# Performance work log

Hardware: AMD Instinct MI355X
Metric: run time of the kernel (lower is better)

Reference implementation:

```python
import jax, jax.numpy as jnp
import numpy as np

B, T, C = 2, 2048, 1024
H = 16
D = C // H  # head_dim = 64
SCALE = D ** -0.5


def setup_inputs() -> dict:
    key = jax.random.key(0)
    ks = jax.random.split(key, 5)
    s = 0.02
    return {
        "x": jax.random.normal(ks[0], (B, T, C), dtype=jnp.float32),
        "w_qkv": jax.random.normal(ks[1], (C, 3 * C), dtype=jnp.float32) * s,
        "b_qkv": jnp.zeros((3 * C,), dtype=jnp.float32),
        "w_proj": jax.random.normal(ks[2], (C, C), dtype=jnp.float32) * s,
        "b_proj": jnp.zeros((C,), dtype=jnp.float32),
    }


def reference(x, w_qkv, b_qkv, w_proj, b_proj):
    Bx, Tx, Cx = x.shape
    qkv = x @ w_qkv + b_qkv                      # [B,T,3C]
    q, k, v = jnp.split(qkv, 3, axis=-1)
    # [B,T,C] -> [B,H,T,D]
    q = q.reshape(Bx, Tx, H, D).transpose(0, 2, 1, 3)
    k = k.reshape(Bx, Tx, H, D).transpose(0, 2, 1, 3)
    v = v.reshape(Bx, Tx, H, D).transpose(0, 2, 1, 3)
    attn = jnp.einsum('bhqd,bhkd->bhqk', q, k) * SCALE
    causal = jnp.tril(jnp.ones((Tx, Tx), dtype=bool))
    attn = jnp.where(causal[None, None], attn, -jnp.inf)
    attn = jax.nn.softmax(attn, axis=-1)
    out = jnp.einsum('bhqk,bhkd->bhqd', attn, v)  # [B,H,T,D]
    out = out.transpose(0, 2, 1, 3).reshape(Bx, Tx, Cx)
    return out @ w_proj + b_proj
```

## Files before the change

### kernel.cpp

```cpp
#include <hip/hip_runtime.h>
#include <hip/hip_bf16.h>
#include <math.h>

#define T_SEQ 2048
#define NHEAD 16
#define HDIM  64
#define CDIM  1024
#define KDIM  1024
#define SCALE_L2E 0.1803368801111204f

typedef __attribute__((ext_vector_type(8))) short bf16x8;
typedef __attribute__((ext_vector_type(4))) float f32x4;
typedef __attribute__((ext_vector_type(16))) float f32x16;
typedef __attribute__((ext_vector_type(8))) unsigned short u16x8;
typedef __attribute__((ext_vector_type(4))) unsigned int u32x4;

__device__ __forceinline__ unsigned short f2bf(float f) {
    unsigned int u = __builtin_bit_cast(unsigned int, f);
    u += 0x7fffu + ((u >> 16) & 1u);
    return (unsigned short)(u >> 16);
}
__device__ __forceinline__ unsigned int cvt_pk_bf16(float lo, float hi_) {
    unsigned int r;
    asm("v_cvt_pk_bf16_f32 %0, %1, %2" : "=v"(r) : "v"(lo), "v"(hi_));
    return r;
}
__device__ __forceinline__ void pl32swap(unsigned int &a, unsigned int &b) {
    asm("v_permlane32_swap_b32 %0, %1" : "+v"(a), "+v"(b));
}
__device__ __forceinline__ float exp2_fast(float x) {
    float r; asm("v_exp_f32 %0, %1" : "=v"(r) : "v"(x)); return r;
}
__device__ __forceinline__ void gld16(const unsigned short* g, unsigned short* l) {
    __builtin_amdgcn_global_load_lds(
        (const __attribute__((address_space(1))) unsigned int*)g,
        (__attribute__((address_space(3))) unsigned int*)l,
        16, 0, 0);
}

__global__ __launch_bounds__(256) void prep_all(
    const float* __restrict__ x,  unsigned short* __restrict__ Xb,
    const float* __restrict__ wq, unsigned short* __restrict__ Wqt,
    const float* __restrict__ wp, unsigned short* __restrict__ Wpt)
{
    __shared__ unsigned short Ls[64][72];
    const int bid = blockIdx.x;
    if (bid < 2048) {
        size_t i = ((size_t)bid * 256 + threadIdx.x) * 8;
        float4 a = *(const float4*)(x + i);
        float4 b = *(const float4*)(x + i + 4);
        u32x4 o;
        o[0] = cvt_pk_bf16(a.x, a.y);
        o[1] = cvt_pk_bf16(a.z, a.w);
        o[2] = cvt_pk_bf16(b.x, b.y);
        o[3] = cvt_pk_bf16(b.z, b.w);
        *(u32x4*)(Xb + i) = o;
        return;
    }
    const float* W; unsigned short* Wt; int NC, n0, k0;
    if (bid < 2048 + 768) {
        int b = bid - 2048;
        W = wq; Wt = Wqt; NC = 3072; n0 = (b % 48) * 64; k0 = (b / 48) * 64;
    } else {
        int b = bid - 2816;
        W = wp; Wt = Wpt; NC = 1024; n0 = (b % 16) * 64; k0 = (b / 16) * 64;
    }
    const int t = threadIdx.x;
    {
        int kr = t >> 2, nc = (t & 3) * 16;
        #pragma unroll
        for (int j = 0; j < 4; j++) {
            float4 v = *(const float4*)(W + (size_t)(k0 + kr) * NC + n0 + nc + j * 4);
            Ls[nc + j*4 + 0][kr] = f2bf(v.x);
            Ls[nc + j*4 + 1][kr] = f2bf(v.y);
            Ls[nc + j*4 + 2][kr] = f2bf(v.z);
            Ls[nc + j*4 + 3][kr] = f2bf(v.w);
        }
    }
    __syncthreads();
    {
        int nr = t >> 2, kc = (t & 3) * 16;
        u16x8 o0 = *(const u16x8*)&Ls[nr][kc];
        u16x8 o1 = *(const u16x8*)&Ls[nr][kc + 8];
        *(u16x8*)(Wt + (size_t)(n0 + nr) * KDIM + k0 + kc)     = o0;
        *(u16x8*)(Wt + (size_t)(n0 + nr) * KDIM + k0 + kc + 8) = o1;
    }
}

template<int NC, int EPI>
__global__ __launch_bounds__(256) void gemm_k(
    const unsigned short* __restrict__ A, const unsigned short* __restrict__ Wt,
    const float* __restrict__ bias, float* __restrict__ Of,
    unsigned short* __restrict__ Qb, unsigned short* __restrict__ Kb,
    unsigned short* __restrict__ Vt)
{
    __shared__ unsigned short As[128 * 64];
    __shared__ unsigned short Bs[128 * 64];

    const int tid  = threadIdx.x;
    const int lane = tid & 63;
    const int wid  = tid >> 6;
    const int m0 = blockIdx.x * 128;
    const int n0 = blockIdx.y * 128;
    const int wm = (wid >> 1) * 64;
    const int wn = (wid & 1) * 64;
    const int rl = lane & 15;

    const int r8 = lane >> 3, s8 = lane & 7;
    const int swzs = (s8 ^ r8) * 8;

    f32x4 acc[4][4] = {};

    for (int k0 = 0; k0 < KDIM; k0 += 64) {
        #pragma unroll
        for (int c = 0; c < 4; c++) {
            int row = (wid << 5) + (c << 3) + r8;
            gld16(A  + (size_t)(m0 + row) * KDIM + k0 + swzs, &As[(size_t)((wid<<5)+(c<<3)) * 64]);
            gld16(Wt + (size_t)(n0 + row) * KDIM + k0 + swzs, &Bs[(size_t)((wid<<5)+(c<<3)) * 64]);
        }
        __syncthreads();
        #pragma unroll
        for (int kc = 0; kc < 2; kc++) {
            const int sb = kc * 4 + (lane >> 4);
            bf16x8 af[4], bfr[4];
            #pragma unroll
            for (int f = 0; f < 4; f++) {
                int sw = (sb ^ (rl & 7)) * 8;
                af[f]  = *(const bf16x8*)&As[(wm + f*16 + rl) * 64 + sw];
                bfr[f] = *(const bf16x8*)&Bs[(wn + f*16 + rl) * 64 + sw];
            }
            __builtin_amdgcn_s_setprio(1);
            #pragma unroll
            for (int i = 0; i < 4; i++)
                #pragma unroll
                for (int j = 0; j < 4; j++)
                    acc[i][j] = __builtin_amdgcn_mfma_f32_16x16x32_bf16(af[i], bfr[j], acc[i][j], 0, 0, 0);
            __builtin_amdgcn_s_setprio(0);
        }
        __syncthreads();
    }

    #pragma unroll
    for (int j = 0; j < 4; j++) {
        int gn = n0 + wn + j*16 + rl;
        float bv = bias[gn];
        #pragma unroll
        for (int i = 0; i < 4; i++) {
            int gm0 = m0 + wm + i*16 + (lane >> 4) * 4;
            #pragma unroll
            for (int r = 0; r < 4; r++) {
                float v = acc[i][j][r] + bv;
                int gm = gm0 + r;
                if (EPI == 0) {
                    int which = gn >> 10;
                    int cw = gn & 1023;
                    int h = cw >> 6, d = cw & 63;
                    int b = gm >> 11, t = gm & 2047;
                    size_t bh = (size_t)(b * NHEAD + h);
                    if (which == 0)      Qb[(bh * T_SEQ + t) * HDIM + d] = f2bf(v * SCALE_L2E);
                    else if (which == 1) Kb[(bh * T_SEQ + t) * HDIM + d] = f2bf(v);
                    else                 Vt[(bh * HDIM + d) * T_SEQ + t] = f2bf(v);
                } else {
                    Of[(size_t)gm * NC + gn] = v;
                }
            }
        }
    }
}

__global__ __launch_bounds__(256, 4) void attn_k(
    const unsigned short* __restrict__ Qb, const unsigned short* __restrict__ Kb,
    const unsigned short* __restrict__ Vt, unsigned short* __restrict__ AO)
{
    __shared__ unsigned short sbuf[4 * 4096];
    __shared__ float mlbuf[2 * 64];

    const int tid  = threadIdx.x;
    const int lane = tid & 63;
    const int w    = tid >> 6;
    const int pair = w >> 1;
    const int par  = w & 1;
    const int bh   = blockIdx.x;
    const int by   = blockIdx.y;
    const int qt   = pair ? (63 - by) : by;
    const int ql   = lane & 31;
    const int hi   = lane >> 5;
    const int qg   = (qt << 5) + ql;

    const unsigned short* Qp = Qb + (size_t)bh * T_SEQ * HDIM;
    const unsigned short* Kp = Kb + (size_t)bh * T_SEQ * HDIM;
    const unsigned short* Vp = Vt + (size_t)bh * HDIM * T_SEQ;

    unsigned short* kbuf = sbuf + w * 4096;
    const char* kbB = (const char*)kbuf;
    const char* vbB = (const char*)(kbuf + 2048);

    const int r8 = lane >> 3, s8 = lane & 7;
    const int key = s8 ^ r8;
    const unsigned short* kSrc = Kp + (size_t)r8 * HDIM + (key << 3);
    const unsigned short* vSrc = Vp + (size_t)((key >> 2) * 32 + r8) * T_SEQ + (key & 3) * 8;

    auto issue_tile = [&](int t) {
        #pragma unroll
        for (int c = 0; c < 4; c++)
            gld16(kSrc + ((size_t)t << 11) + (c << 9), kbuf + (c << 9));
        #pragma unroll
        for (int c = 0; c < 4; c++)
            gld16(vSrc + ((size_t)c << 14) + (t << 5), kbuf + 2048 + (c << 9));
    };

    bf16x8 qf[4];
    #pragma unroll
    for (int dc = 0; dc < 4; dc++)
        qf[dc] = *(const bf16x8*)(Qp + (size_t)qg * HDIM + dc*16 + hi*8);

    float l_run = 0.f;
    f32x16 o0 = {}, o1 = {};

    if (par <= qt) {
        issue_tile(par);
        for (int t = par; t <= qt; t += 2) {
            asm volatile("s_waitcnt vmcnt(0)" ::: "memory");
            __builtin_amdgcn_sched_barrier(0);

            bf16x8 kf[4];
            #pragma unroll
            for (int dc = 0; dc < 4; dc++)
                kf[dc] = *(const bf16x8*)(kbB + ql*128 + (((dc << 1 | hi) ^ (ql & 7)) << 4));
            bf16x8 v00 = *(const bf16x8*)(vbB + ql*128 + (((0 + hi) ^ (ql & 7)) << 4));
            bf16x8 v01 = *(const bf16x8*)(vbB + ql*128 + (((2 + hi) ^ (ql & 7)) << 4));
            bf16x8 v10 = *(const bf16x8*)(vbB + ql*128 + (((4 + hi) ^ (ql & 7)) << 4));
            bf16x8 v11 = *(const bf16x8*)(vbB + ql*128 + (((6 + hi) ^ (ql & 7)) << 4));
            asm volatile("s_waitcnt lgkmcnt(0)" ::: "memory");
            __builtin_amdgcn_sched_barrier(0);

            if (t + 2 <= qt) issue_tile(t + 2);

            f32x16 s = {};
            __builtin_amdgcn_s_setprio(1);
            #pragma unroll
            for (int dc = 0; dc < 4; dc++)
                s = __builtin_amdgcn_mfma_f32_32x32x16_bf16(kf[dc], qf[dc], s, 0, 0, 0);
            __builtin_amdgcn_s_setprio(0);

            float p[16];
            if (t == qt) {
                #pragma unroll
                for (int r = 0; r < 16; r++) {
                    int kv = (t << 5) + (r & 3) + 8 * (r >> 2) + 4 * hi;
                    p[r] = (kv > qg) ? 0.f : exp2_fast(s[r]);
                }
            } else {
                #pragma unroll
                for (int r = 0; r < 16; r++) p[r] = exp2_fast(s[r]);
            }
            float r0 = (p[0]  + p[1])  + (p[2]  + p[3]);
            float r1 = (p[4]  + p[5])  + (p[6]  + p[7]);
            float r2 = (p[8]  + p[9])  + (p[10] + p[11]);
            float r3 = (p[12] + p[13]) + (p[14] + p[15]);
            l_run += (r0 + r1) + (r2 + r3);

            unsigned int c[8];
            #pragma unroll
            for (int i = 0; i < 8; i++) c[i] = cvt_pk_bf16(p[2*i], p[2*i+1]);
            pl32swap(c[0], c[2]);  pl32swap(c[1], c[3]);
            pl32swap(c[4], c[6]);  pl32swap(c[5], c[7]);
            u32x4 b0 = {c[0], c[1], c[2], c[3]};
            u32x4 b1 = {c[4], c[5], c[6], c[7]};
            bf16x8 pf0 = __builtin_bit_cast(bf16x8, b0);
            bf16x8 pf1 = __builtin_bit_cast(bf16x8, b1);

            __builtin_amdgcn_s_setprio(1);
            o0 = __builtin_amdgcn_mfma_f32_32x32x16_bf16(v00, pf0, o0, 0, 0, 0);
            o0 = __builtin_amdgcn_mfma_f32_32x32x16_bf16(v01, pf1, o0, 0, 0, 0);
            o1 = __builtin_amdgcn_mfma_f32_32x32x16_bf16(v10, pf0, o1, 0, 0, 0);
            o1 = __builtin_amdgcn_mfma_f32_32x32x16_bf16(v11, pf1, o1, 0, 0, 0);
            __builtin_amdgcn_s_setprio(0);
        }
    }

    __syncthreads();
    float* plf = (float*)(sbuf + pair * 8192);
    if (par == 1) {
        #pragma unroll
        for (int j = 0; j < 4; j++) {
            f32x4 a = { o0[4*j], o0[4*j+1], o0[4*j+2], o0[4*j+3] };
            *(f32x4*)(plf + (size_t)(j*64 + lane) * 4) = a;
        }
        #pragma unroll
        for (int j = 0; j < 4; j++) {
            f32x4 a = { o1[4*j], o1[4*j+1], o1[4*j+2], o1[4*j+3] };
            *(f32x4*)(plf + (size_t)((4+j)*64 + lane) * 4) = a;
        }
        mlbuf[pair * 64 + lane] = l_run;
    }
    __syncthreads();
    if (par == 0) {
        float l_all = l_run + mlbuf[pair * 64 + lane];
        l_all += __shfl_xor(l_all, 32);
        float linv = 1.f / l_all;
        const int b = bh >> 4, h = bh & 15;
        unsigned short* aop = AO + ((size_t)(b * T_SEQ + qg)) * CDIM + h * HDIM;
        #pragma unroll
        for (int qd = 0; qd < 4; qd++) {
            f32x4 x0 = *(const f32x4*)(plf + (size_t)(qd*64 + lane) * 4);
            f32x4 x1 = *(const f32x4*)(plf + (size_t)((4+qd)*64 + lane) * 4);
            uint2 w0, w1;
            w0.x = cvt_pk_bf16((o0[4*qd+0] + x0[0]) * linv, (o0[4*qd+1] + x0[1]) * linv);
            w0.y = cvt_pk_bf16((o0[4*qd+2] + x0[2]) * linv, (o0[4*qd+3] + x0[3]) * linv);
            w1.x = cvt_pk_bf16((o1[4*qd+0] + x1[0]) * linv, (o1[4*qd+1] + x1[1]) * linv);
            w1.y = cvt_pk_bf16((o1[4*qd+2] + x1[2]) * linv, (o1[4*qd+3] + x1[3]) * linv);
            *(uint2*)(aop + qd*8 + hi*4)      = w0;
            *(uint2*)(aop + 32 + qd*8 + hi*4) = w1;
        }
    }
}

extern "C" void kernel_launch(void* const* d_in, const int* in_sizes, int n_in,
                              void* d_out, int out_size, void* d_ws, size_t ws_size,
                              hipStream_t stream) {
    const float* x      = (const float*)d_in[0];
    const float* w_qkv  = (const float*)d_in[1];
    const float* b_qkv  = (const float*)d_in[2];
    const float* w_proj = (const float*)d_in[3];
    const float* b_proj = (const float*)d_in[4];
    float* out = (float*)d_out;

    const size_t MI = (size_t)1 << 20;
    unsigned short* base = (unsigned short*)d_ws;
    unsigned short* Qb  = base;
    unsigned short* Kb  = base + 4*MI;
    unsigned short* Vt  = base + 8*MI;
    unsigned short* Wqt = base + 12*MI;
    unsigned short* Wpt = base + 15*MI;
    unsigned short* Xb  = base + 16*MI;
    unsigned short* AO  = Xb;

    prep_all<<<dim3(3072), 256, 0, stream>>>(x, Xb, w_qkv, Wqt, w_proj, Wpt);
    gemm_k<3072, 0><<<dim3(32, 24), 256, 0, stream>>>(
        Xb, Wqt, b_qkv, nullptr, Qb, Kb, Vt);
    attn_k<<<dim3(32, 32), 256, 0, stream>>>(Qb, Kb, Vt, AO);
    gemm_k<1024, 1><<<dim3(32, 8), 256, 0, stream>>>(
        AO, Wpt, b_proj, out, nullptr, nullptr, nullptr);
}
```

Before: 105.1 us.

## Share each K/V tile across both paired query tiles with four-way KV split

Each wave now holds Q fragments for both query tiles (qa and 63-qa) and iterates over every fourth KV tile, computing scores for both query tiles from the same K/V fragments held in registers. Each K/V tile is loaded once per block instead of once per query tile, which cuts global and LDS traffic. In exchange the four waves' partial outputs are reduced through shared memory in two extra rounds, register pressure rises (launch bounds lowered to 3), and wave load balance differs.

```diff
diff --git a/kernel.cpp b/kernel.cpp
--- a/kernel.cpp
+++ b/kernel.cpp
@@ -168,24 +168,24 @@
     }
 }
 
-__global__ __launch_bounds__(256, 4) void attn_k(
+__global__ __launch_bounds__(256, 3) void attn_k(
     const unsigned short* __restrict__ Qb, const unsigned short* __restrict__ Kb,
     const unsigned short* __restrict__ Vt, unsigned short* __restrict__ AO)
 {
     __shared__ unsigned short sbuf[4 * 4096];
-    __shared__ float mlbuf[2 * 64];
+    __shared__ float mlbuf[3 * 64];
 
     const int tid  = threadIdx.x;
     const int lane = tid & 63;
     const int w    = tid >> 6;
-    const int pair = w >> 1;
-    const int par  = w & 1;
     const int bh   = blockIdx.x;
     const int by   = blockIdx.y;
-    const int qt   = pair ? (63 - by) : by;
+    const int qa   = by;
+    const int qb   = 63 - by;
     const int ql   = lane & 31;
     const int hi   = lane >> 5;
-    const int qg   = (qt << 5) + ql;
+    const int qgA  = (qa << 5) + ql;
+    const int qgB  = (qb << 5) + ql;
 
     const unsigned short* Qp = Qb + (size_t)bh * T_SEQ * HDIM;
     const unsigned short* Kp = Kb + (size_t)bh * T_SEQ * HDIM;
@@ -209,46 +209,47 @@
             gld16(vSrc + ((size_t)c << 14) + (t << 5), kbuf + 2048 + (c << 9));
     };
 
-    bf16x8 qf[4];
+    bf16x8 qfA[4], qfB[4];
     #pragma unroll
-    for (int dc = 0; dc < 4; dc++)
-        qf[dc] = *(const bf16x8*)(Qp + (size_t)qg * HDIM + dc*16 + hi*8);
-
-    float l_run = 0.f;
-    f32x16 o0 = {}, o1 = {};
-
-    if (par <= qt) {
-        issue_tile(par);
-        for (int t = par; t <= qt; t += 2) {
-            asm volatile("s_waitcnt vmcnt(0)" ::: "memory");
-            __builtin_amdgcn_sched_barrier(0);
-
-            bf16x8 kf[4];
-            #pragma unroll
-            for (int dc = 0; dc < 4; dc++)
-                kf[dc] = *(const bf16x8*)(kbB + ql*128 + (((dc << 1 | hi) ^ (ql & 7)) << 4));
-            bf16x8 v00 = *(const bf16x8*)(vbB + ql*128 + (((0 + hi) ^ (ql & 7)) << 4));
-            bf16x8 v01 = *(const bf16x8*)(vbB + ql*128 + (((2 + hi) ^ (ql & 7)) << 4));
-            bf16x8 v10 = *(const bf16x8*)(vbB + ql*128 + (((4 + hi) ^ (ql & 7)) << 4));
-            bf16x8 v11 = *(const bf16x8*)(vbB + ql*128 + (((6 + hi) ^ (ql & 7)) << 4));
-            asm volatile("s_waitcnt lgkmcnt(0)" ::: "memory");
-            __builtin_amdgcn_sched_barrier(0);
-
-            if (t + 2 <= qt) issue_tile(t + 2);
-
+    for (int dc = 0; dc < 4; dc++) {
+        qfA[dc] = *(const bf16x8*)(Qp + (size_t)qgA * HDIM + dc*16 + hi*8);
+        qfB[dc] = *(const bf16x8*)(Qp + (size_t)qgB * HDIM + dc*16 + hi*8);
+    }
+
+    float lA = 0.f, lB = 0.f;
+    f32x16 oA0 = {}, oA1 = {}, oB0 = {}, oB1 = {};
+
+    issue_tile(w);
+    for (int t = w; t <= qb; t += 4) {
+        asm volatile("s_waitcnt vmcnt(0)" ::: "memory");
+        __builtin_amdgcn_sched_barrier(0);
+
+        bf16x8 kf[4];
+        #pragma unroll
+        for (int dc = 0; dc < 4; dc++)
+            kf[dc] = *(const bf16x8*)(kbB + ql*128 + (((dc << 1 | hi) ^ (ql & 7)) << 4));
+        bf16x8 v00 = *(const bf16x8*)(vbB + ql*128 + (((0 + hi) ^ (ql & 7)) << 4));
+        bf16x8 v01 = *(const bf16x8*)(vbB + ql*128 + (((2 + hi) ^ (ql & 7)) << 4));
+        bf16x8 v10 = *(const bf16x8*)(vbB + ql*128 + (((4 + hi) ^ (ql & 7)) << 4));
+        bf16x8 v11 = *(const bf16x8*)(vbB + ql*128 + (((6 + hi) ^ (ql & 7)) << 4));
+        asm volatile("s_waitcnt lgkmcnt(0)" ::: "memory");
+        __builtin_amdgcn_sched_barrier(0);
+
+        if (t + 4 <= qb) issue_tile(t + 4);
+
+        if (t <= qa) {
             f32x16 s = {};
             __builtin_amdgcn_s_setprio(1);
             #pragma unroll
             for (int dc = 0; dc < 4; dc++)
-                s = __builtin_amdgcn_mfma_f32_32x32x16_bf16(kf[dc], qf[dc], s, 0, 0, 0);
+                s = __builtin_amdgcn_mfma_f32_32x32x16_bf16(kf[dc], qfA[dc], s, 0, 0, 0);
             __builtin_amdgcn_s_setprio(0);
-
             float p[16];
-            if (t == qt) {
+            if (t == qa) {
                 #pragma unroll
                 for (int r = 0; r < 16; r++) {
                     int kv = (t << 5) + (r & 3) + 8 * (r >> 2) + 4 * hi;
-                    p[r] = (kv > qg) ? 0.f : exp2_fast(s[r]);
+                    p[r] = (kv > qgA) ? 0.f : exp2_fast(s[r]);
                 }
             } else {
                 #pragma unroll
@@ -258,8 +259,7 @@
             float r1 = (p[4]  + p[5])  + (p[6]  + p[7]);
             float r2 = (p[8]  + p[9])  + (p[10] + p[11]);
             float r3 = (p[12] + p[13]) + (p[14] + p[15]);
-            l_run += (r0 + r1) + (r2 + r3);
-
+            lA += (r0 + r1) + (r2 + r3);
             unsigned int c[8];
             #pragma unroll
             for (int i = 0; i < 8; i++) c[i] = cvt_pk_bf16(p[2*i], p[2*i+1]);
@@ -269,47 +269,137 @@
             u32x4 b1 = {c[4], c[5], c[6], c[7]};
             bf16x8 pf0 = __builtin_bit_cast(bf16x8, b0);
             bf16x8 pf1 = __builtin_bit_cast(bf16x8, b1);
-
             __builtin_amdgcn_s_setprio(1);
-            o0 = __builtin_amdgcn_mfma_f32_32x32x16_bf16(v00, pf0, o0, 0, 0, 0);
-            o0 = __builtin_amdgcn_mfma_f32_32x32x16_bf16(v01, pf1, o0, 0, 0, 0);
-            o1 = __builtin_amdgcn_mfma_f32_32x32x16_bf16(v10, pf0, o1, 0, 0, 0);
-            o1 = __builtin_amdgcn_mfma_f32_32x32x16_bf16(v11, pf1, o1, 0, 0, 0);
+            oA0 = __builtin_amdgcn_mfma_f32_32x32x16_bf16(v00, pf0, oA0, 0, 0, 0);
+            oA0 = __builtin_amdgcn_mfma_f32_32x32x16_bf16(v01, pf1, oA0, 0, 0, 0);
+            oA1 = __builtin_amdgcn_mfma_f32_32x32x16_bf16(v10, pf0, oA1, 0, 0, 0);
+            oA1 = __builtin_amdgcn_mfma_f32_32x32x16_bf16(v11, pf1, oA1, 0, 0, 0);
             __builtin_amdgcn_s_setprio(0);
         }
-    }
-
+
+        {
+            f32x16 s = {};
+            __builtin_amdgcn_s_setprio(1);
+            #pragma unroll
+            for (int dc = 0; dc < 4; dc++)
+                s = __builtin_amdgcn_mfma_f32_32x32x16_bf16(kf[dc], qfB[dc], s, 0, 0, 0);
+            __builtin_amdgcn_s_setprio(0);
+            float p[16];
+            if (t == qb) {
+                #pragma unroll
+                for (int r = 0; r < 16; r++) {
+                    int kv = (t << 5) + (r & 3) + 8 * (r >> 2) + 4 * hi;
+                    p[r] = (kv > qgB) ? 0.f : exp2_fast(s[r]);
+                }
+            } else {
+                #pragma unroll
+                for (int r = 0; r < 16; r++) p[r] = exp2_fast(s[r]);
+            }
+            float r0 = (p[0]  + p[1])  + (p[2]  + p[3]);
+            float r1 = (p[4]  + p[5])  + (p[6]  + p[7]);
+            float r2 = (p[8]  + p[9])  + (p[10] + p[11]);
+            float r3 = (p[12] + p[13]) + (p[14] + p[15]);
+            lB += (r0 + r1) + (r2 + r3);
+            unsigned int c[8];
+            #pragma unroll
+            for (int i = 0; i < 8; i++) c[i] = cvt_pk_bf16(p[2*i], p[2*i+1]);
+            pl32swap(c[0], c[2]);  pl32swap(c[1], c[3]);
+            pl32swap(c[4], c[6]);  pl32swap(c[5], c[7]);
+            u32x4 b0 = {c[0], c[1], c[2], c[3]};
+            u32x4 b1 = {c[4], c[5], c[6], c[7]};
+            bf16x8 pf0 = __builtin_bit_cast(bf16x8, b0);
+            bf16x8 pf1 = __builtin_bit_cast(bf16x8, b1);
+            __builtin_amdgcn_s_setprio(1);
+            oB0 = __builtin_amdgcn_mfma_f32_32x32x16_bf16(v00, pf0, oB0, 0, 0, 0);
+            oB0 = __builtin_amdgcn_mfma_f32_32x32x16_bf16(v01, pf1, oB0, 0, 0, 0);
+            oB1 = __builtin_amdgcn_mfma_f32_32x32x16_bf16(v10, pf0, oB1, 0, 0, 0);
+            oB1 = __builtin_amdgcn_mfma_f32_32x32x16_bf16(v11, pf1, oB1, 0, 0, 0);
+            __builtin_amdgcn_s_setprio(0);
+        }
+    }
+
+    const int b = bh >> 4, h = bh & 15;
+    float* lf = (float*)sbuf;
     __syncthreads();
-    float* plf = (float*)(sbuf + pair * 8192);
-    if (par == 1) {
+    if (w > 0) {
+        float* reg = lf + (size_t)(w - 1) * 2048;
         #pragma unroll
         for (int j = 0; j < 4; j++) {
-            f32x4 a = { o0[4*j], o0[4*j+1], o0[4*j+2], o0[4*j+3] };
-            *(f32x4*)(plf + (size_t)(j*64 + lane) * 4) = a;
+            f32x4 a = { oA0[4*j], oA0[4*j+1], oA0[4*j+2], oA0[4*j+3] };
+            *(f32x4*)(reg + (size_t)(j*64 + lane) * 4) = a;
         }
         #pragma unroll
         for (int j = 0; j < 4; j++) {
-            f32x4 a = { o1[4*j], o1[4*j+1], o1[4*j+2], o1[4*j+3] };
-            *(f32x4*)(plf + (size_t)((4+j)*64 + lane) * 4) = a;
-        }
-        mlbuf[pair * 64 + lane] = l_run;
+            f32x4 a = { oA1[4*j], oA1[4*j+1], oA1[4*j+2], oA1[4*j+3] };
+            *(f32x4*)(reg + (size_t)((4+j)*64 + lane) * 4) = a;
+        }
+        mlbuf[(w - 1) * 64 + lane] = lA;
     }
     __syncthreads();
-    if (par == 0) {
-        float l_all = l_run + mlbuf[pair * 64 + lane];
-        l_all += __shfl_xor(l_all, 32);
-        float linv = 1.f / l_all;
-        const int b = bh >> 4, h = bh & 15;
-        unsigned short* aop = AO + ((size_t)(b * T_SEQ + qg)) * CDIM + h * HDIM;
+    if (w == 0) {
+        float lt = lA + mlbuf[lane] + mlbuf[64 + lane] + mlbuf[128 + lane];
+        lt += __shfl_xor(lt, 32);
+        float linv = 1.f / lt;
+        unsigned short* aop = AO + ((size_t)(b * T_SEQ + qgA)) * CDIM + h * HDIM;
         #pragma unroll
         for (int qd = 0; qd < 4; qd++) {
-            f32x4 x0 = *(const f32x4*)(plf + (size_t)(qd*64 + lane) * 4);
-            f32x4 x1 = *(const f32x4*)(plf + (size_t)((4+qd)*64 + lane) * 4);
+            f32x4 x1a = *(const f32x4*)(lf + (size_t)(qd*64 + lane) * 4);
+            f32x4 x1b = *(const f32x4*)(lf + (size_t)((4+qd)*64 + lane) * 4);
+            f32x4 x2a = *(const f32x4*)(lf + 2048 + (size_t)(qd*64 + lane) * 4);
+            f32x4 x2b = *(const f32x4*)(lf + 2048 + (size_t)((4+qd)*64 + lane) * 4);
+            f32x4 x3a = *(const f32x4*)(lf + 4096 + (size_t)(qd*64 + lane) * 4);
+            f32x4 x3b = *(const f32x4*)(lf + 4096 + (size_t)((4+qd)*64 + lane) * 4);
             uint2 w0, w1;
-            w0.x = cvt_pk_bf16((o0[4*qd+0] + x0[0]) * linv, (o0[4*qd+1] + x0[1]) * linv);
-            w0.y = cvt_pk_bf16((o0[4*qd+2] + x0[2]) * linv, (o0[4*qd+3] + x0[3]) * linv);
-            w1.x = cvt_pk_bf16((o1[4*qd+0] + x1[0]) * linv, (o1[4*qd+1] + x1[1]) * linv);
-            w1.y = cvt_pk_bf16((o1[4*qd+2] + x1[2]) * linv, (o1[4*qd+3] + x1[3]) * linv);
+            w0.x = cvt_pk_bf16((oA0[4*qd+0] + x1a[0] + x2a[0] + x3a[0]) * linv,
+                               (oA0[4*qd+1] + x1a[1] + x2a[1] + x3a[1]) * linv);
+            w0.y = cvt_pk_bf16((oA0[4*qd+2] + x1a[2] + x2a[2] + x3a[2]) * linv,
+                               (oA0[4*qd+3] + x1a[3] + x2a[3] + x3a[3]) * linv);
+            w1.x = cvt_pk_bf16((oA1[4*qd+0] + x1b[0] + x2b[0] + x3b[0]) * linv,
+                               (oA1[4*qd+1] + x1b[1] + x2b[1] + x3b[1]) * linv);
+            w1.y = cvt_pk_bf16((oA1[4*qd+2] + x1b[2] + x2b[2] + x3b[2]) * linv,
+                               (oA1[4*qd+3] + x1b[3] + x2b[3] + x3b[3]) * linv);
+            *(uint2*)(aop + qd*8 + hi*4)      = w0;
+            *(uint2*)(aop + 32 + qd*8 + hi*4) = w1;
+        }
+    }
+    __syncthreads();
+    if (w > 0) {
+        float* reg = lf + (size_t)(w - 1) * 2048;
+        #pragma unroll
+        for (int j = 0; j < 4; j++) {
+            f32x4 a = { oB0[4*j], oB0[4*j+1], oB0[4*j+2], oB0[4*j+3] };
+            *(f32x4*)(reg + (size_t)(j*64 + lane) * 4) = a;
+        }
+        #pragma unroll
+        for (int j = 0; j < 4; j++) {
+            f32x4 a = { oB1[4*j], oB1[4*j+1], oB1[4*j+2], oB1[4*j+3] };
+            *(f32x4*)(reg + (size_t)((4+j)*64 + lane) * 4) = a;
+        }
+        mlbuf[(w - 1) * 64 + lane] = lB;
+    }
+    __syncthreads();
+    if (w == 0) {
+        float lt = lB + mlbuf[lane] + mlbuf[64 + lane] + mlbuf[128 + lane];
+        lt += __shfl_xor(lt, 32);
+        float linv = 1.f / lt;
+        unsigned short* aop = AO + ((size_t)(b * T_SEQ + qgB)) * CDIM + h * HDIM;
+        #pragma unroll
+        for (int qd = 0; qd < 4; qd++) {
+            f32x4 x1a = *(const f32x4*)(lf + (size_t)(qd*64 + lane) * 4);
+            f32x4 x1b = *(const f32x4*)(lf + (size_t)((4+qd)*64 + lane) * 4);
+            f32x4 x2a = *(const f32x4*)(lf + 2048 + (size_t)(qd*64 + lane) * 4);
+            f32x4 x2b = *(const f32x4*)(lf + 2048 + (size_t)((4+qd)*64 + lane) * 4);
+            f32x4 x3a = *(const f32x4*)(lf + 4096 + (size_t)(qd*64 + lane) * 4);
+            f32x4 x3b = *(const f32x4*)(lf + 4096 + (size_t)((4+qd)*64 + lane) * 4);
+            uint2 w0, w1;
+            w0.x = cvt_pk_bf16((oB0[4*qd+0] + x1a[0] + x2a[0] + x3a[0]) * linv,
+                               (oB0[4*qd+1] + x1a[1] + x2a[1] + x3a[1]) * linv);
+            w0.y = cvt_pk_bf16((oB0[4*qd+2] + x1a[2] + x2a[2] + x3a[2]) * linv,
+                               (oB0[4*qd+3] + x1a[3] + x2a[3] + x3a[3]) * linv);
+            w1.x = cvt_pk_bf16((oB1[4*qd+0] + x1b[0] + x2b[0] + x3b[0]) * linv,
+                               (oB1[4*qd+1] + x1b[1] + x2b[1] + x3b[1]) * linv);
+            w1.y = cvt_pk_bf16((oB1[4*qd+2] + x1b[2] + x2b[2] + x3b[2]) * linv,
+                               (oB1[4*qd+3] + x1b[3] + x2b[3] + x3b[3]) * linv);
             *(uint2*)(aop + qd*8 + hi*4)      = w0;
             *(uint2*)(aop + 32 + qd*8 + hi*4) = w1;
         }
```

New measurement: 113.6 us. 8.1% more time.

## Use 256x256 double-buffered tile GEMM for QKV projection

Applied to the files above, without the earlier changes.

Replaces the 128x128 QKV GEMM with a dedicated 512-thread kernel computing 256x256 tiles, with two LDS stages prefetched via async global loads and explicit vmcnt waits. The goal is higher operand reuse per block and overlap of global loads with MFMA work. The grid shrinks to 192 blocks, which may leave compute units idle and raises register and LDS pressure. The output projection GEMM is simplified to a non-templated kernel.

```diff
diff --git a/kernel.cpp b/kernel.cpp
--- a/kernel.cpp
+++ b/kernel.cpp
@@ -87,13 +87,107 @@
     }
 }
 
-template<int NC, int EPI>
-__global__ __launch_bounds__(256) void gemm_k(
+__global__ __launch_bounds__(512, 2) void gemm256_k(
     const unsigned short* __restrict__ A, const unsigned short* __restrict__ Wt,
-    const float* __restrict__ bias, float* __restrict__ Of,
+    const float* __restrict__ bias,
     unsigned short* __restrict__ Qb, unsigned short* __restrict__ Kb,
     unsigned short* __restrict__ Vt)
 {
+    __shared__ unsigned short As[2 * 16384];
+    __shared__ unsigned short Bs[2 * 16384];
+
+    const int tid  = threadIdx.x;
+    const int lane = tid & 63;
+    const int wid  = tid >> 6;
+    const int m0 = blockIdx.x * 256;
+    const int n0 = blockIdx.y * 256;
+    const int wm = (wid >> 2) * 128;
+    const int wn = (wid & 3) * 64;
+    const int rl = lane & 15;
+
+    const int r8 = lane >> 3, s8 = lane & 7;
+    const int swzs = (s8 ^ r8) * 8;
+
+    auto stage = [&](int t) {
+        const int buf = (t & 1) * 16384;
+        const int k0 = t << 6;
+        #pragma unroll
+        for (int c = 0; c < 4; c++) {
+            int row = (wid << 5) + (c << 3) + r8;
+            int dst = buf + ((wid << 5) + (c << 3)) * 64;
+            gld16(A  + (size_t)(m0 + row) * KDIM + k0 + swzs, &As[dst]);
+            gld16(Wt + (size_t)(n0 + row) * KDIM + k0 + swzs, &Bs[dst]);
+        }
+    };
+
+    f32x4 acc[8][4] = {};
+
+    auto compute = [&](int t) {
+        const int buf = (t & 1) * 16384;
+        #pragma unroll
+        for (int kc = 0; kc < 2; kc++) {
+            const int sb = kc * 4 + (lane >> 4);
+            const int sw = (sb ^ (rl & 7)) * 8;
+            bf16x8 af[8], bfr[4];
+            #pragma unroll
+            for (int f = 0; f < 8; f++)
+                af[f]  = *(const bf16x8*)&As[buf + (wm + f*16 + rl) * 64 + sw];
+            #pragma unroll
+            for (int g = 0; g < 4; g++)
+                bfr[g] = *(const bf16x8*)&Bs[buf + (wn + g*16 + rl) * 64 + sw];
+            __builtin_amdgcn_s_setprio(1);
+            #pragma unroll
+            for (int i = 0; i < 8; i++)
+                #pragma unroll
+                for (int j = 0; j < 4; j++)
+                    acc[i][j] = __builtin_amdgcn_mfma_f32_16x16x32_bf16(af[i], bfr[j], acc[i][j], 0, 0, 0);
+            __builtin_amdgcn_s_setprio(0);
+        }
+    };
+
+    stage(0);
+    stage(1);
+    for (int t = 0; t < 16; t++) {
+        if (t < 15) asm volatile("s_waitcnt vmcnt(8)" ::: "memory");
+        else        asm volatile("s_waitcnt vmcnt(0)" ::: "memory");
+        __builtin_amdgcn_s_barrier();
+        __builtin_amdgcn_sched_barrier(0);
+        compute(t);
+        asm volatile("s_waitcnt lgkmcnt(0)" ::: "memory");
+        __builtin_amdgcn_sched_barrier(0);
+        __builtin_amdgcn_s_barrier();
+        if (t + 2 < 16) stage(t + 2);
+    }
+
+    const int which = n0 >> 10;
+    #pragma unroll
+    for (int j = 0; j < 4; j++) {
+        int gn = n0 + wn + j*16 + rl;
+        float bv = bias[gn];
+        int cw = gn & 1023;
+        int h = cw >> 6, d = cw & 63;
+        #pragma unroll
+        for (int i = 0; i < 8; i++) {
+            int gm0 = m0 + wm + i*16 + (lane >> 4) * 4;
+            #pragma unroll
+            for (int r = 0; r < 4; r++) {
+                float v = acc[i][j][r] + bv;
+                int gm = gm0 + r;
+                int b = gm >> 11, t = gm & 2047;
+                size_t bh = (size_t)(b * NHEAD + h);
+                if (which == 0)      Qb[(bh * T_SEQ + t) * HDIM + d] = f2bf(v * SCALE_L2E);
+                else if (which == 1) Kb[(bh * T_SEQ + t) * HDIM + d] = f2bf(v);
+                else                 Vt[(bh * HDIM + d) * T_SEQ + t] = f2bf(v);
+            }
+        }
+    }
+}
+
+__global__ __launch_bounds__(256) void gemm_k(
+    const unsigned short* __restrict__ A, const unsigned short* __restrict__ Wt,
+    const float* __restrict__ bias, float* __restrict__ Of)
+{
+    const int NC = 1024;
     __shared__ unsigned short As[128 * 64];
     __shared__ unsigned short Bs[128 * 64];
 
@@ -148,22 +242,8 @@
         for (int i = 0; i < 4; i++) {
             int gm0 = m0 + wm + i*16 + (lane >> 4) * 4;
             #pragma unroll
-            for (int r = 0; r < 4; r++) {
-                float v = acc[i][j][r] + bv;
-                int gm = gm0 + r;
-                if (EPI == 0) {
-                    int which = gn >> 10;
-                    int cw = gn & 1023;
-                    int h = cw >> 6, d = cw & 63;
-                    int b = gm >> 11, t = gm & 2047;
-                    size_t bh = (size_t)(b * NHEAD + h);
-                    if (which == 0)      Qb[(bh * T_SEQ + t) * HDIM + d] = f2bf(v * SCALE_L2E);
-                    else if (which == 1) Kb[(bh * T_SEQ + t) * HDIM + d] = f2bf(v);
-                    else                 Vt[(bh * HDIM + d) * T_SEQ + t] = f2bf(v);
-                } else {
-                    Of[(size_t)gm * NC + gn] = v;
-                }
-            }
+            for (int r = 0; r < 4; r++)
+                Of[(size_t)(gm0 + r) * NC + gn] = acc[i][j][r] + bv;
         }
     }
 }
@@ -337,9 +417,8 @@
     unsigned short* AO  = Xb;
 
     prep_all<<<dim3(3072), 256, 0, stream>>>(x, Xb, w_qkv, Wqt, w_proj, Wpt);
-    gemm_k<3072, 0><<<dim3(32, 24), 256, 0, stream>>>(
-        Xb, Wqt, b_qkv, nullptr, Qb, Kb, Vt);
+    gemm256_k<<<dim3(16, 12), 512, 0, stream>>>(
+        Xb, Wqt, b_qkv, Qb, Kb, Vt);
     attn_k<<<dim3(32, 32), 256, 0, stream>>>(Qb, Kb, Vt, AO);
-    gemm_k<1024, 1><<<dim3(32, 8), 256, 0, stream>>>(
-        AO, Wpt, b_proj, out, nullptr, nullptr, nullptr);
-}
+    gemm_k<<<dim3(32, 8), 256, 0, stream>>>(AO, Wpt, b_proj, out);
+}
```

Result: slower. 130.0 us (+23.7%).
